# Performance work log

Hardware: AMD Instinct MI355X
Metric: run time of the kernel (lower is better)

## Reference

```python
import jax, jax.numpy as jnp
import numpy as np

B, T, D, U = 32, 2048, 512, 512

def setup_inputs() -> dict:
    key = jax.random.key(0)
    ks = jax.random.split(key, 8)
    s = 0.02
    return {
        "query": jax.random.normal(ks[0], (B, D), dtype=jnp.float32),
        "values": jax.random.normal(ks[1], (B, T, D), dtype=jnp.float32),
        "W1_w": jax.random.normal(ks[2], (D, U), dtype=jnp.float32) * s,
        "W1_b": jnp.zeros((U,), dtype=jnp.float32),
        "W2_w": jax.random.normal(ks[3], (D, U), dtype=jnp.float32) * s,
        "W2_b": jnp.zeros((U,), dtype=jnp.float32),
        "V_w": jax.random.normal(ks[4], (U, 1), dtype=jnp.float32) * s,
        "V_b": jnp.zeros((1,), dtype=jnp.float32),
    }

def reference(query, values, W1_w, W1_b, W2_w, W2_b, V_w, V_b):
    # query: [B, D] -> [B, 1, U]; values: [B, T, D] -> [B, T, U]
    q_proj = (query @ W1_w + W1_b)[:, None, :]              # [B, 1, U]
    v_proj = jnp.einsum('btd,du->btu', values, W2_w) + W2_b  # [B, T, U]
    score = jnp.tanh(q_proj + v_proj) @ V_w + V_b            # [B, T, 1]
    attn = jax.nn.softmax(score, axis=1)                     # [B, T, 1]
    context = jnp.sum(attn * values, axis=1)                 # [B, D]
    return context, attn
```

## Files before the change

kernel.cpp:

```cpp
#include <hip/hip_runtime.h>
#include <hip/hip_bf16.h>
#include <cstddef>
#include <cstdint>

#define B_ 32
#define T_ 2048
#define D_ 512
#define U_ 512

typedef __attribute__((ext_vector_type(8))) short bf16x8;
typedef __attribute__((ext_vector_type(4))) float f32x4;

__device__ __forceinline__ unsigned short f2bf(float f) {
  union { float f; unsigned u; } x; x.f = f;
  unsigned r = x.u + 0x7fffu + ((x.u >> 16) & 1u);
  return (unsigned short)(r >> 16);
}
__device__ __forceinline__ float tanh_fast(float x) {
  float e = __expf(2.0f * x);
  return 1.0f - 2.0f * __builtin_amdgcn_rcpf(e + 1.0f);
}

__device__ __forceinline__ void wave0_sumabs_vw(const float* __restrict__ Vw,
                                                float* Cs, int tid) {
  if (tid < 64) {
    float c = 0.f;
    #pragma unroll
    for (int i = 0; i < 8; ++i) c += fabsf(Vw[tid + i * 64]);
    c += __shfl_xor(c, 1);  c += __shfl_xor(c, 2);  c += __shfl_xor(c, 4);
    c += __shfl_xor(c, 8);  c += __shfl_xor(c, 16); c += __shfl_xor(c, 32);
    if (tid == 0) *Cs = c;
  }
}

__global__ void kA_prep(const float* __restrict__ W2, unsigned* __restrict__ W2P,
                        const float* __restrict__ query, const float* __restrict__ W1,
                        const float* __restrict__ W1b, const float* __restrict__ W2b,
                        float* __restrict__ qp, float* __restrict__ ctx) {
  const int tid = threadIdx.x;
  if (blockIdx.x < 16) {
    const int kg = blockIdx.x;
    __shared__ unsigned short w2s[32][514];
    const float4* W2v = (const float4*)(W2 + (size_t)kg * 32 * U_);
    #pragma unroll
    for (int i = 0; i < 16; ++i) {
      int idx = i * 256 + tid;
      float4 v = W2v[idx];
      int r = idx >> 7, c = (idx & 127) * 4;
      w2s[r][c + 0] = f2bf(v.x); w2s[r][c + 1] = f2bf(v.y);
      w2s[r][c + 2] = f2bf(v.z); w2s[r][c + 3] = f2bf(v.w);
    }
    __syncthreads();
    const int lq = tid >> 6, lr = (tid >> 2) & 15, j = tid & 3;
    const int kb = lq * 8 + j * 2;
    #pragma unroll
    for (int ut = 0; ut < 32; ++ut)
      W2P[ut * 4096 + kg * 256 + tid] =
          (unsigned)w2s[kb][ut * 16 + lr] | ((unsigned)w2s[kb + 1][ut * 16 + lr] << 16);
  } else {
    __shared__ float qs[D_];
    const int blk = blockIdx.x - 16;
    const int b = blk >> 1, uhh = (blk & 1) * 256;
    qs[tid] = query[b * D_ + tid];
    qs[tid + 256] = query[b * D_ + tid + 256];
    __syncthreads();
    const int u = uhh + tid;
    float a0 = 0, a1 = 0, a2 = 0, a3 = 0, a4 = 0, a5 = 0, a6 = 0, a7 = 0;
    for (int d = 0; d < D_; d += 8) {
      a0 += qs[d + 0] * W1[(size_t)(d + 0) * U_ + u];
      a1 += qs[d + 1] * W1[(size_t)(d + 1) * U_ + u];
      a2 += qs[d + 2] * W1[(size_t)(d + 2) * U_ + u];
      a3 += qs[d + 3] * W1[(size_t)(d + 3) * U_ + u];
      a4 += qs[d + 4] * W1[(size_t)(d + 4) * U_ + u];
      a5 += qs[d + 5] * W1[(size_t)(d + 5) * U_ + u];
      a6 += qs[d + 6] * W1[(size_t)(d + 6) * U_ + u];
      a7 += qs[d + 7] * W1[(size_t)(d + 7) * U_ + u];
    }
    qp[b * U_ + u] = ((a0 + a1) + (a2 + a3)) + ((a4 + a5) + (a6 + a7)) + W1b[u] + W2b[u];
    const int gt = blk * 256 + tid;
    ctx[gt] = 0.0f;
  }
}

__global__ __launch_bounds__(512, 4) void k2attn(
    const float* __restrict__ values, const unsigned short* __restrict__ W2P,
    const float* __restrict__ qp, const float* __restrict__ Vw,
    float* __restrict__ score, float* __restrict__ ctxU) {
  __shared__ __align__(16) float avb[4][1024];
  __shared__ float sred[8][32];
  __shared__ float ps2[32];
  __shared__ float Cs;

  const int tid = threadIdx.x;
  const int bx = blockIdx.x;
  const int m0 = bx * 32;
  const int b = m0 >> 11;
  const int l = tid & 63, w = tid >> 6;
  const int lr = l & 15, lq = l >> 4;

  const int row_st = w * 4 + (l >> 4);
  const int fseg = l & 15;
  const float* vrow = values + (size_t)(m0 + row_st) * D_ + fseg * 4;

  f32x4 acc[2][4];
  #pragma unroll
  for (int mi = 0; mi < 2; ++mi)
    #pragma unroll
    for (int ni = 0; ni < 4; ++ni) acc[mi][ni] = (f32x4){0.f, 0.f, 0.f, 0.f};

  const unsigned short* Bb = W2P + (size_t)(w * 4) * 8192 + (size_t)l * 8;

  auto consume = [&](float4 g, int s) {
    __hip_bfloat162 h0 = __float22bfloat162_rn(make_float2(g.x, g.y));
    __hip_bfloat162 h1 = __float22bfloat162_rn(make_float2(g.z, g.w));
    union { __hip_bfloat162 h; unsigned u; } c0, c1; c0.h = h0; c1.h = h1;
    int slot = (fseg >> 1) ^ (row_st & 7);
    char* dst = (char*)avb[s & 3] + row_st * 128 + (slot << 4) + ((fseg & 1) << 3);
    *(uint2*)dst = make_uint2(c0.u, c1.u);
  };

  wave0_sumabs_vw(Vw, &Cs, tid);

  float4 Ga = *(const float4*)(vrow);
  float4 Gb = *(const float4*)(vrow + 64);
  float4 Gc = *(const float4*)(vrow + 128);
  consume(Ga, 0);
  consume(Gb, 1);
  __syncthreads();
  const float C = Cs;
  float4 Gcons = Gc;

  #pragma unroll
  for (int e = 0; e < 8; ++e) {
    float4 Gnew = (float4){0.f, 0.f, 0.f, 0.f};
    if (e < 5) Gnew = *(const float4*)(vrow + (e + 3) * 64);
    const char* buf = (const char*)avb[e & 3];
    #pragma unroll
    for (int kq = 0; kq < 2; ++kq) {
      const int kg = e * 2 + kq;
      const int sl = ((kq << 2) | lq) ^ (lr & 7);
      bf16x8 a0 = *(const bf16x8*)(buf + (lr) * 128 + (sl << 4));
      bf16x8 a1 = *(const bf16x8*)(buf + (16 + lr) * 128 + (sl << 4));
      bf16x8 b0 = *(const bf16x8*)(Bb + 0 * 8192 + (size_t)kg * 512);
      bf16x8 b1 = *(const bf16x8*)(Bb + 1 * 8192 + (size_t)kg * 512);
      bf16x8 b2 = *(const bf16x8*)(Bb + 2 * 8192 + (size_t)kg * 512);
      bf16x8 b3 = *(const bf16x8*)(Bb + 3 * 8192 + (size_t)kg * 512);
      __builtin_amdgcn_s_setprio(1);
      acc[0][0] = __builtin_amdgcn_mfma_f32_16x16x32_bf16(a0, b0, acc[0][0], 0, 0, 0);
      acc[1][0] = __builtin_amdgcn_mfma_f32_16x16x32_bf16(a1, b0, acc[1][0], 0, 0, 0);
      acc[0][1] = __builtin_amdgcn_mfma_f32_16x16x32_bf16(a0, b1, acc[0][1], 0, 0, 0);
      acc[1][1] = __builtin_amdgcn_mfma_f32_16x16x32_bf16(a1, b1, acc[1][1], 0, 0, 0);
      acc[0][2] = __builtin_amdgcn_mfma_f32_16x16x32_bf16(a0, b2, acc[0][2], 0, 0, 0);
      acc[1][2] = __builtin_amdgcn_mfma_f32_16x16x32_bf16(a1, b2, acc[1][2], 0, 0, 0);
      acc[0][3] = __builtin_amdgcn_mfma_f32_16x16x32_bf16(a0, b3, acc[0][3], 0, 0, 0);
      acc[1][3] = __builtin_amdgcn_mfma_f32_16x16x32_bf16(a1, b3, acc[1][3], 0, 0, 0);
      __builtin_amdgcn_s_setprio(0);
      if (kq == 0 && e < 6) consume(Gcons, e + 2);
    }
    Gcons = Gnew;
    __builtin_amdgcn_sched_barrier(0);
    asm volatile("s_waitcnt lgkmcnt(0)" ::: "memory");
    __builtin_amdgcn_s_barrier();
    __builtin_amdgcn_sched_barrier(0);
  }

  float sacc[2][4];
  #pragma unroll
  for (int mi = 0; mi < 2; ++mi)
    #pragma unroll
    for (int r = 0; r < 4; ++r) sacc[mi][r] = 0.0f;
  #pragma unroll
  for (int ni = 0; ni < 4; ++ni) {
    int u = (w * 4 + ni) * 16 + lr;
    float qpv = qp[b * U_ + u], vv = Vw[u];
    #pragma unroll
    for (int mi = 0; mi < 2; ++mi)
      #pragma unroll
      for (int r = 0; r < 4; ++r)
        sacc[mi][r] += tanh_fast(acc[mi][ni][r] + qpv) * vv;
  }
  #pragma unroll
  for (int mi = 0; mi < 2; ++mi)
    #pragma unroll
    for (int r = 0; r < 4; ++r) {
      float v = sacc[mi][r];
      v += __shfl_xor(v, 1); v += __shfl_xor(v, 2);
      v += __shfl_xor(v, 4); v += __shfl_xor(v, 8);
      if (lr == 0) sred[w][mi * 16 + lq * 4 + r] = v;
    }
  __syncthreads();

  if (tid < 32) {
    float s = 0.f;
    #pragma unroll
    for (int wv = 0; wv < 8; ++wv) s += sred[wv][tid];
    score[m0 + tid] = s;
    ps2[tid] = __expf(s - C);
  }
  __syncthreads();

  float accc = 0.f;
  const int col = tid;
  #pragma unroll 4
  for (int row = 0; row < 32; ++row)
    accc += ps2[row] * values[(size_t)(m0 + row) * D_ + col];
  atomicAdd(&ctxU[(size_t)b * D_ + col], accc);
}

__global__ void kB_final(const float* __restrict__ Vw, float* __restrict__ attn,
                         float* __restrict__ ctx) {
  __shared__ float Cs;
  __shared__ float red[4];
  const int b = blockIdx.x, tid = threadIdx.x;
  wave0_sumabs_vw(Vw, &Cs, tid);
  __syncthreads();
  const float C = Cs;
  float* s = attn + b * T_;
  float p[8];
  float sum = 0.f;
  #pragma unroll
  for (int i = 0; i < 8; ++i) { p[i] = __expf(s[tid + i * 256] - C); sum += p[i]; }
  #pragma unroll
  for (int off = 1; off < 64; off <<= 1) sum += __shfl_xor(sum, off);
  if ((tid & 63) == 0) red[tid >> 6] = sum;
  __syncthreads();
  sum = (red[0] + red[1]) + (red[2] + red[3]);
  const float inv = 1.0f / sum;
  #pragma unroll
  for (int i = 0; i < 8; ++i) attn[b * T_ + tid + i * 256] = p[i] * inv;
  #pragma unroll
  for (int i = 0; i < 2; ++i) ctx[b * D_ + tid + i * 256] *= inv;
}

extern "C" void kernel_launch(void* const* d_in, const int* in_sizes, int n_in,
                              void* d_out, int out_size, void* d_ws, size_t ws_size,
                              hipStream_t stream) {
  const float* query = (const float*)d_in[0];
  const float* values = (const float*)d_in[1];
  const float* W1w = (const float*)d_in[2];
  const float* W1b = (const float*)d_in[3];
  const float* W2w = (const float*)d_in[4];
  const float* W2b = (const float*)d_in[5];
  const float* Vw  = (const float*)d_in[6];

  float* out = (float*)d_out;
  float* ctx  = out;
  float* attn = out + B_ * D_;
  float* score = attn;

  char* ws = (char*)d_ws;
  unsigned* W2P = (unsigned*)ws;
  float* qp    = (float*)(ws + 512 * 1024);

  kA_prep<<<80, 256, 0, stream>>>(W2w, W2P, query, W1w, W1b, W2b, qp, ctx);
  k2attn<<<2048, 512, 0, stream>>>(values, (const unsigned short*)W2P, qp, Vw, score, ctx);
  kB_final<<<32, 256, 0, stream>>>(Vw, attn, ctx);
}
```

Before: 274.9 us.

## Prefetch W2 fragments two k-steps ahead and halve LDS barriers

W2 bf16 B fragments now go into a three-slot register ring and are loaded two k-steps ahead of the MFMAs that use them, so global-load latency is hidden. The prefetch of values rows deepens by one stage. With the four LDS buffers, the workgroup barrier now runs only every second iteration. This is meant to cut load stalls and sync overhead in the main GEMM loop, at the cost of more VGPRs, which could lower occupancy or cause spills.

```diff
diff --git a/kernel.cpp b/kernel.cpp
--- a/kernel.cpp
+++ b/kernel.cpp
@@ -119,49 +119,59 @@
     *(uint2*)dst = make_uint2(c0.u, c1.u);
   };
 
+  bf16x8 Bf[3][4];
+  auto loadB = [&](int slot, int kappa) {
+    #pragma unroll
+    for (int ni = 0; ni < 4; ++ni)
+      Bf[slot][ni] = *(const bf16x8*)(Bb + (size_t)ni * 8192 + (size_t)kappa * 512);
+  };
+
   wave0_sumabs_vw(Vw, &Cs, tid);
 
-  float4 Ga = *(const float4*)(vrow);
-  float4 Gb = *(const float4*)(vrow + 64);
-  float4 Gc = *(const float4*)(vrow + 128);
-  consume(Ga, 0);
-  consume(Gb, 1);
+  float4 g0 = *(const float4*)(vrow);
+  float4 g1 = *(const float4*)(vrow + 64);
+  float4 g2 = *(const float4*)(vrow + 128);
+  float4 g3 = *(const float4*)(vrow + 192);
+  loadB(0, 0);
+  loadB(1, 1);
+  consume(g0, 0);
+  consume(g1, 1);
   __syncthreads();
   const float C = Cs;
-  float4 Gcons = Gc;
+  float4 Gpend[2];
+  Gpend[0] = g2; Gpend[1] = g3;
 
   #pragma unroll
   for (int e = 0; e < 8; ++e) {
     float4 Gnew = (float4){0.f, 0.f, 0.f, 0.f};
-    if (e < 5) Gnew = *(const float4*)(vrow + (e + 3) * 64);
+    if (e < 4) Gnew = *(const float4*)(vrow + (e + 4) * 64);
     const char* buf = (const char*)avb[e & 3];
     #pragma unroll
     for (int kq = 0; kq < 2; ++kq) {
-      const int kg = e * 2 + kq;
+      const int kappa = e * 2 + kq;
+      if (kappa + 2 < 16) loadB((kappa + 2) % 3, kappa + 2);
       const int sl = ((kq << 2) | lq) ^ (lr & 7);
       bf16x8 a0 = *(const bf16x8*)(buf + (lr) * 128 + (sl << 4));
       bf16x8 a1 = *(const bf16x8*)(buf + (16 + lr) * 128 + (sl << 4));
-      bf16x8 b0 = *(const bf16x8*)(Bb + 0 * 8192 + (size_t)kg * 512);
-      bf16x8 b1 = *(const bf16x8*)(Bb + 1 * 8192 + (size_t)kg * 512);
-      bf16x8 b2 = *(const bf16x8*)(Bb + 2 * 8192 + (size_t)kg * 512);
-      bf16x8 b3 = *(const bf16x8*)(Bb + 3 * 8192 + (size_t)kg * 512);
       __builtin_amdgcn_s_setprio(1);
-      acc[0][0] = __builtin_amdgcn_mfma_f32_16x16x32_bf16(a0, b0, acc[0][0], 0, 0, 0);
-      acc[1][0] = __builtin_amdgcn_mfma_f32_16x16x32_bf16(a1, b0, acc[1][0], 0, 0, 0);
-      acc[0][1] = __builtin_amdgcn_mfma_f32_16x16x32_bf16(a0, b1, acc[0][1], 0, 0, 0);
-      acc[1][1] = __builtin_amdgcn_mfma_f32_16x16x32_bf16(a1, b1, acc[1][1], 0, 0, 0);
-      acc[0][2] = __builtin_amdgcn_mfma_f32_16x16x32_bf16(a0, b2, acc[0][2], 0, 0, 0);
-      acc[1][2] = __builtin_amdgcn_mfma_f32_16x16x32_bf16(a1, b2, acc[1][2], 0, 0, 0);
-      acc[0][3] = __builtin_amdgcn_mfma_f32_16x16x32_bf16(a0, b3, acc[0][3], 0, 0, 0);
-      acc[1][3] = __builtin_amdgcn_mfma_f32_16x16x32_bf16(a1, b3, acc[1][3], 0, 0, 0);
+      acc[0][0] = __builtin_amdgcn_mfma_f32_16x16x32_bf16(a0, Bf[kappa % 3][0], acc[0][0], 0, 0, 0);
+      acc[1][0] = __builtin_amdgcn_mfma_f32_16x16x32_bf16(a1, Bf[kappa % 3][0], acc[1][0], 0, 0, 0);
+      acc[0][1] = __builtin_amdgcn_mfma_f32_16x16x32_bf16(a0, Bf[kappa % 3][1], acc[0][1], 0, 0, 0);
+      acc[1][1] = __builtin_amdgcn_mfma_f32_16x16x32_bf16(a1, Bf[kappa % 3][1], acc[1][1], 0, 0, 0);
+      acc[0][2] = __builtin_amdgcn_mfma_f32_16x16x32_bf16(a0, Bf[kappa % 3][2], acc[0][2], 0, 0, 0);
+      acc[1][2] = __builtin_amdgcn_mfma_f32_16x16x32_bf16(a1, Bf[kappa % 3][2], acc[1][2], 0, 0, 0);
+      acc[0][3] = __builtin_amdgcn_mfma_f32_16x16x32_bf16(a0, Bf[kappa % 3][3], acc[0][3], 0, 0, 0);
+      acc[1][3] = __builtin_amdgcn_mfma_f32_16x16x32_bf16(a1, Bf[kappa % 3][3], acc[1][3], 0, 0, 0);
       __builtin_amdgcn_s_setprio(0);
-      if (kq == 0 && e < 6) consume(Gcons, e + 2);
-    }
-    Gcons = Gnew;
-    __builtin_amdgcn_sched_barrier(0);
-    asm volatile("s_waitcnt lgkmcnt(0)" ::: "memory");
-    __builtin_amdgcn_s_barrier();
-    __builtin_amdgcn_sched_barrier(0);
+      if (kq == 0 && e < 6) consume(Gpend[0], e + 2);
+    }
+    Gpend[0] = Gpend[1]; Gpend[1] = Gnew;
+    if (e & 1) {
+      __builtin_amdgcn_sched_barrier(0);
+      asm volatile("s_waitcnt lgkmcnt(0)" ::: "memory");
+      __builtin_amdgcn_s_barrier();
+      __builtin_amdgcn_sched_barrier(0);
+    }
   }
 
   float sacc[2][4];
```

After: 267.4 us. 2.7% less time.
